# Performance work log

Measured on AMD Instinct MI355X. Metric: run time of the kernel, lower is better.

The kernel has to match this reference:

```python
import jax, jax.numpy as jnp
import numpy as np

B, C, N_IN = 32, 64, 10475
N_OUT = 2619
NNZ = 8 * N_OUT  # ~8 barycentric entries per output vertex


def setup_inputs() -> dict:
    key = jax.random.key(0)
    k1, k2, k3, k4 = jax.random.split(key, 4)
    x = jax.random.normal(k1, (B, C, N_IN), dtype=jnp.float32)
    # Sparse mesh-sampling operator M [N_OUT, N_IN] in COO form,
    # sparsity pattern shared across the whole batch.
    M_rows = jax.random.randint(k2, (NNZ,), 0, N_OUT, dtype=jnp.int32)
    M_cols = jax.random.randint(k3, (NNZ,), 0, N_IN, dtype=jnp.int32)
    M_vals = jax.random.uniform(k4, (NNZ,), dtype=jnp.float32)
    return {"x": x, "M_rows": M_rows, "M_cols": M_cols, "M_vals": M_vals}


def reference(x, M_rows, M_cols, M_vals):
    """Batched spmm: out[b, c, r] = sum_{k: M_rows[k]==r} M_vals[k] * x[b, c, M_cols[k]].

    Equivalent to the torch module: for each batch element, M @ x[b].T, stacked,
    then transposed back to [B, C, N_OUT]. Here the batch loop is fused into a
    single gather + segment_sum that reuses the shared sparsity pattern.
    """
    # Gather source vertex features for every nnz entry: [B, C, NNZ]
    g = x[:, :, M_cols] * M_vals
    # segment_sum reduces over the leading axis -> move nnz to front
    g = jnp.moveaxis(g, 2, 0)                                   # [NNZ, B, C]
    out = jax.ops.segment_sum(g, M_rows, num_segments=N_OUT)    # [N_OUT, B, C]
    return jnp.moveaxis(out, 0, 2)                              # [B, C, N_OUT]
```

## Files before the change

kernel.cpp:

```cpp
#include <hip/hip_runtime.h>
#include <stdint.h>

#define Bdim   32
#define Cdim   64
#define N_IN   10475
#define N_OUT  2619
#define NNZ    (8 * N_OUT)
#define MAIN_BLK 512
#define CHUNK  41
#define SMALL_BLK 256
#define Gpair  2
#define NBLK   (Bdim * Cdim / Gpair)

#define SENT_META 0x03FFC000u

#define OFF_OFFS   10480
#define OFF_ENT    20976
#define OFF_ELAST  (OFF_ENT + 20 * MAIN_BLK * 16)
#define WS_NEEDED  (OFF_ELAST + MAIN_BLK * 8)
#define ENT_U2     ((WS_NEEDED - OFF_ENT) / 8)

__global__ __launch_bounds__(SMALL_BLK) void init_ws(
        int* __restrict__ cursor, uint2* __restrict__ ent2) {
    int i = blockIdx.x * SMALL_BLK + threadIdx.x;
    if (i < N_OUT) cursor[i] = 0;
    if (i < ENT_U2) ent2[i] = make_uint2(SENT_META, 0u);
}

__global__ __launch_bounds__(SMALL_BLK) void hist_rows(
        const int* __restrict__ rows, int* __restrict__ counts) {
    int k = blockIdx.x * SMALL_BLK + threadIdx.x;
    if (k < NNZ) atomicAdd(&counts[rows[k]], 1);
}

__global__ __launch_bounds__(1024) void scan_counts(
        int* __restrict__ counts, int* __restrict__ offsets) {
    __shared__ int wsum[16];
    const int t = threadIdx.x, lane = t & 63, w = t >> 6;
    const int base = t * 3;
    int v0 = (base + 0 < N_OUT) ? counts[base + 0] : 0;
    int v1 = (base + 1 < N_OUT) ? counts[base + 1] : 0;
    int v2 = (base + 2 < N_OUT) ? counts[base + 2] : 0;
    int s = v0 + v1 + v2;
    const int tot = s;
    #pragma unroll
    for (int d = 1; d < 64; d <<= 1) {
        int n = __shfl_up(s, d);
        if (lane >= d) s += n;
    }
    if (lane == 63) wsum[w] = s;
    __syncthreads();
    if (t < 16) {
        int ws_ = wsum[t];
        #pragma unroll
        for (int d = 1; d < 16; d <<= 1) {
            int n = __shfl_up(ws_, d);
            if (t >= d) ws_ += n;
        }
        wsum[t] = ws_;
    }
    __syncthreads();
    int excl = ((w > 0) ? wsum[w - 1] : 0) + (s - tot);
    if (base + 0 <= N_OUT) { offsets[base + 0] = excl; if (base + 0 < N_OUT) counts[base + 0] = excl; }
    excl += v0;
    if (base + 1 <= N_OUT) { offsets[base + 1] = excl; if (base + 1 < N_OUT) counts[base + 1] = excl; }
    excl += v1;
    if (base + 2 <= N_OUT) { offsets[base + 2] = excl; if (base + 2 < N_OUT) counts[base + 2] = excl; }
}

__global__ __launch_bounds__(SMALL_BLK) void scatter_entries(
        const int* __restrict__ rows, const int* __restrict__ cols,
        const float* __restrict__ vals,
        int* __restrict__ cursor, const int* __restrict__ offsets,
        uint2* __restrict__ ent2, uint2* __restrict__ entLast) {
    int k = blockIdx.x * SMALL_BLK + threadIdx.x;
    if (k < NNZ) {
        int r = rows[k];
        int p = atomicAdd(&cursor[r], 1);
        uint32_t flag = (p == offsets[r + 1] - 1) ? 0x80000000u : 0u;
        uint32_t meta = flag | ((uint32_t)r << 14) | (uint32_t)cols[k];
        uint2 e = make_uint2(meta, __float_as_uint(vals[k]));
        int t = p / CHUNK;
        int s = p - t * CHUNK;
        if (s < 40) ent2[(s >> 1) * (MAIN_BLK * 2) + t * 2 + (s & 1)] = e;
        else        entLast[t] = e;
    }
}

__global__ __launch_bounds__(MAIN_BLK) void spmm_g2(
        const float* __restrict__ x,
        const uint4* __restrict__ ent4,
        const uint2* __restrict__ entLast,
        float* __restrict__ out) {
    __shared__ uint32_t xs[N_IN];
    __shared__ float2   out2[N_OUT];
    __shared__ int      wCarryRow[8];
    __shared__ float    wC0[8], wC1[8];

    const int blk  = blockIdx.x;
    const int t    = threadIdx.x, lane = t & 63, w = t >> 6;
    const float* __restrict__ xr0 = x + (size_t)(Gpair * blk) * N_IN;
    const float* __restrict__ xr1 = xr0 + N_IN;

    #pragma unroll 4
    for (int i = t; i < N_IN; i += MAIN_BLK) {
        uint32_t a = __float_as_uint(xr0[i]);
        uint32_t b = __float_as_uint(xr1[i]);
        uint32_t lo = (a + 0x7FFFu + ((a >> 16) & 1u)) >> 16;
        uint32_t hi = (b + 0x7FFFu + ((b >> 16) & 1u)) & 0xFFFF0000u;
        xs[i] = lo | hi;
    }
    #pragma unroll
    for (int i = t; i < N_OUT; i += MAIN_BLK) out2[i] = make_float2(0.f, 0.f);
    __syncthreads();

    float acc0 = 0.f, acc1 = 0.f, f0 = 0.f, f1 = 0.f;
    int firstRow = -1;

#define FEED(meta, vb) do {                                              \
        uint32_t xp = xs[(meta) & 0x3FFFu];                              \
        float v = __uint_as_float(vb);                                   \
        acc0 = fmaf(v, __uint_as_float(xp << 16), acc0);                 \
        acc1 = fmaf(v, __uint_as_float(xp & 0xFFFF0000u), acc1);         \
        if ((int)(meta) < 0) {                                           \
            int row_ = (int)(((meta) >> 14) & 0xFFFu);                   \
            if (firstRow < 0) { firstRow = row_; f0 = acc0; f1 = acc1; } \
            else out2[row_] = make_float2(acc0, acc1);                   \
            acc0 = 0.f; acc1 = 0.f;                                      \
        }                                                                \
    } while (0)

    #pragma unroll
    for (int jb = 0; jb < 5; ++jb) {
        uint4 q0 = ent4[(jb * 4 + 0) * MAIN_BLK + t];
        uint4 q1 = ent4[(jb * 4 + 1) * MAIN_BLK + t];
        uint4 q2 = ent4[(jb * 4 + 2) * MAIN_BLK + t];
        uint4 q3 = ent4[(jb * 4 + 3) * MAIN_BLK + t];
        FEED(q0.x, q0.y); FEED(q0.z, q0.w);
        FEED(q1.x, q1.y); FEED(q1.z, q1.w);
        FEED(q2.x, q2.y); FEED(q2.z, q2.w);
        FEED(q3.x, q3.y); FEED(q3.z, q3.w);
    }
    uint2 el = entLast[t];
    FEED(el.x, el.y);
#undef FEED

    const int   carryRow = (int)((el.x >> 14) & 0xFFFu);
    const float c0 = acc0, c1 = acc1;

    int   pRow = __shfl_up(carryRow, 1);
    float p0   = __shfl_up(c0, 1);
    float p1   = __shfl_up(c1, 1);
    if (lane == 63) { wCarryRow[w] = carryRow; wC0[w] = c0; wC1[w] = c1; }
    __syncthreads();
    if (lane == 0) {
        pRow = (w > 0) ? wCarryRow[w - 1] : -1;
        p0   = (w > 0) ? wC0[w - 1] : 0.f;
        p1   = (w > 0) ? wC1[w - 1] : 0.f;
    }

    if (firstRow >= 0 && firstRow < N_OUT) {
        bool m = (pRow == firstRow);
        out2[firstRow] = make_float2(f0 + (m ? p0 : 0.f),
                                     f1 + (m ? p1 : 0.f));
    }
    __syncthreads();

    float* __restrict__ o0 = out + (size_t)(Gpair * blk) * N_OUT;
    float* __restrict__ o1 = o0 + N_OUT;
    #pragma unroll
    for (int i = t; i < N_OUT; i += MAIN_BLK) {
        float2 vv = out2[i];
        o0[i] = vv.x;
        o1[i] = vv.y;
    }
}

__global__ __launch_bounds__(SMALL_BLK) void spmm_raw(
        const float* __restrict__ x,
        const int* __restrict__ rows,
        const int* __restrict__ cols,
        const float* __restrict__ vals,
        float* __restrict__ out) {
    __shared__ float x_lds[N_IN];
    __shared__ float out_lds[N_OUT];
    const int bc = blockIdx.x;
    const float* __restrict__ xrow = x + (size_t)bc * N_IN;
    for (int i = threadIdx.x; i < N_IN; i += SMALL_BLK) x_lds[i] = xrow[i];
    for (int i = threadIdx.x; i < N_OUT; i += SMALL_BLK) out_lds[i] = 0.0f;
    __syncthreads();
    for (int k = threadIdx.x; k < NNZ; k += SMALL_BLK) {
        atomicAdd(&out_lds[rows[k]], vals[k] * x_lds[cols[k]]);
    }
    __syncthreads();
    float* __restrict__ orow = out + (size_t)bc * N_OUT;
    for (int i = threadIdx.x; i < N_OUT; i += SMALL_BLK) orow[i] = out_lds[i];
}

extern "C" void kernel_launch(void* const* d_in, const int* in_sizes, int n_in,
                              void* d_out, int out_size, void* d_ws, size_t ws_size,
                              hipStream_t stream) {
    const float* x    = (const float*)d_in[0];
    const int*   rows = (const int*)d_in[1];
    const int*   cols = (const int*)d_in[2];
    const float* vals = (const float*)d_in[3];
    float*       out  = (float*)d_out;

    if (ws_size >= (size_t)WS_NEEDED) {
        char*  ws      = (char*)d_ws;
        int*   cursor  = (int*)ws;
        int*   offsets = (int*)(ws + OFF_OFFS);
        uint2* ent2    = (uint2*)(ws + OFF_ENT);
        const uint4* ent4 = (const uint4*)(ws + OFF_ENT);
        uint2* entLast = (uint2*)(ws + OFF_ELAST);

        const int gi = (ENT_U2 + SMALL_BLK - 1) / SMALL_BLK;
        const int gk = (NNZ + SMALL_BLK - 1) / SMALL_BLK;

        init_ws<<<gi, SMALL_BLK, 0, stream>>>(cursor, ent2);
        hist_rows<<<gk, SMALL_BLK, 0, stream>>>(rows, cursor);
        scan_counts<<<1, 1024, 0, stream>>>(cursor, offsets);
        scatter_entries<<<gk, SMALL_BLK, 0, stream>>>(rows, cols, vals, cursor,
                                                      offsets, ent2, entLast);
        spmm_g2<<<NBLK, MAIN_BLK, 0, stream>>>(x, ent4, entLast, out);
    } else {
        spmm_raw<<<Bdim * Cdim, SMALL_BLK, 0, stream>>>(x, rows, cols, vals, out);
    }
}
```

Baseline: 159.3 us.

## Write spmm rows straight to global and fix chunk-boundary carries with atomics

The output staging buffer in shared memory is dropped. Completed rows are stored directly to global memory, and each thread's trailing partial row is merged with a global atomicAdd after a block barrier. This replaces the shuffle and shared-memory carry fix-up. The change cuts LDS use to roughly the x tile, allowing a launch bound of 6 blocks per CU. Entries now encode the column as a byte offset so the LDS address needs no shift, and the next group of entries is prefetched while the current one is consumed. The cost is scattered, uncoalesced global stores and an extra global zeroing pass, in exchange for higher occupancy and less LDS traffic.

```diff
diff --git a/kernel.cpp b/kernel.cpp
--- a/kernel.cpp
+++ b/kernel.cpp
@@ -12,7 +12,7 @@
 #define Gpair  2
 #define NBLK   (Bdim * Cdim / Gpair)
 
-#define SENT_META 0x03FFC000u
+#define SENT_META 0x0FFF0000u
 
 #define OFF_OFFS   10480
 #define OFF_ENT    20976
@@ -78,7 +78,7 @@
         int r = rows[k];
         int p = atomicAdd(&cursor[r], 1);
         uint32_t flag = (p == offsets[r + 1] - 1) ? 0x80000000u : 0u;
-        uint32_t meta = flag | ((uint32_t)r << 14) | (uint32_t)cols[k];
+        uint32_t meta = flag | ((uint32_t)r << 16) | ((uint32_t)cols[k] << 2);
         uint2 e = make_uint2(meta, __float_as_uint(vals[k]));
         int t = p / CHUNK;
         int s = p - t * CHUNK;
@@ -87,20 +87,25 @@
     }
 }
 
-__global__ __launch_bounds__(MAIN_BLK) void spmm_g2(
+__global__ __launch_bounds__(MAIN_BLK, 6) void spmm_g2d(
         const float* __restrict__ x,
         const uint4* __restrict__ ent4,
         const uint2* __restrict__ entLast,
         float* __restrict__ out) {
     __shared__ uint32_t xs[N_IN];
-    __shared__ float2   out2[N_OUT];
-    __shared__ int      wCarryRow[8];
-    __shared__ float    wC0[8], wC1[8];
-
-    const int blk  = blockIdx.x;
-    const int t    = threadIdx.x, lane = t & 63, w = t >> 6;
+
+    const int blk = blockIdx.x;
+    const int t   = threadIdx.x;
     const float* __restrict__ xr0 = x + (size_t)(Gpair * blk) * N_IN;
     const float* __restrict__ xr1 = xr0 + N_IN;
+    float* __restrict__ o0 = out + (size_t)(Gpair * blk) * N_OUT;
+    float* __restrict__ o1 = o0 + N_OUT;
+
+    uint4 c0 = ent4[0 * MAIN_BLK + t];
+    uint4 c1 = ent4[1 * MAIN_BLK + t];
+    uint4 c2 = ent4[2 * MAIN_BLK + t];
+    uint4 c3 = ent4[3 * MAIN_BLK + t];
+    const uint2 el = entLast[t];
 
     #pragma unroll 4
     for (int i = t; i < N_IN; i += MAIN_BLK) {
@@ -111,68 +116,47 @@
         xs[i] = lo | hi;
     }
     #pragma unroll
-    for (int i = t; i < N_OUT; i += MAIN_BLK) out2[i] = make_float2(0.f, 0.f);
-    __syncthreads();
-
-    float acc0 = 0.f, acc1 = 0.f, f0 = 0.f, f1 = 0.f;
-    int firstRow = -1;
+    for (int i = t; i < N_OUT; i += MAIN_BLK) { o0[i] = 0.f; o1[i] = 0.f; }
+    __syncthreads();
+
+    float acc0 = 0.f, acc1 = 0.f;
 
 #define FEED(meta, vb) do {                                              \
-        uint32_t xp = xs[(meta) & 0x3FFFu];                              \
+        uint32_t xp = *(const uint32_t*)((const char*)xs + ((meta) & 0xFFFFu)); \
         float v = __uint_as_float(vb);                                   \
         acc0 = fmaf(v, __uint_as_float(xp << 16), acc0);                 \
         acc1 = fmaf(v, __uint_as_float(xp & 0xFFFF0000u), acc1);         \
         if ((int)(meta) < 0) {                                           \
-            int row_ = (int)(((meta) >> 14) & 0xFFFu);                   \
-            if (firstRow < 0) { firstRow = row_; f0 = acc0; f1 = acc1; } \
-            else out2[row_] = make_float2(acc0, acc1);                   \
+            int row_ = (int)(((meta) >> 16) & 0xFFFu);                   \
+            o0[row_] = acc0;                                             \
+            o1[row_] = acc1;                                             \
             acc0 = 0.f; acc1 = 0.f;                                      \
         }                                                                \
     } while (0)
 
     #pragma unroll
     for (int jb = 0; jb < 5; ++jb) {
-        uint4 q0 = ent4[(jb * 4 + 0) * MAIN_BLK + t];
-        uint4 q1 = ent4[(jb * 4 + 1) * MAIN_BLK + t];
-        uint4 q2 = ent4[(jb * 4 + 2) * MAIN_BLK + t];
-        uint4 q3 = ent4[(jb * 4 + 3) * MAIN_BLK + t];
-        FEED(q0.x, q0.y); FEED(q0.z, q0.w);
-        FEED(q1.x, q1.y); FEED(q1.z, q1.w);
-        FEED(q2.x, q2.y); FEED(q2.z, q2.w);
-        FEED(q3.x, q3.y); FEED(q3.z, q3.w);
-    }
-    uint2 el = entLast[t];
+        uint4 n0, n1, n2, n3;
+        if (jb < 4) {
+            n0 = ent4[((jb + 1) * 4 + 0) * MAIN_BLK + t];
+            n1 = ent4[((jb + 1) * 4 + 1) * MAIN_BLK + t];
+            n2 = ent4[((jb + 1) * 4 + 2) * MAIN_BLK + t];
+            n3 = ent4[((jb + 1) * 4 + 3) * MAIN_BLK + t];
+        }
+        FEED(c0.x, c0.y); FEED(c0.z, c0.w);
+        FEED(c1.x, c1.y); FEED(c1.z, c1.w);
+        FEED(c2.x, c2.y); FEED(c2.z, c2.w);
+        FEED(c3.x, c3.y); FEED(c3.z, c3.w);
+        if (jb < 4) { c0 = n0; c1 = n1; c2 = n2; c3 = n3; }
+    }
     FEED(el.x, el.y);
 #undef FEED
 
-    const int   carryRow = (int)((el.x >> 14) & 0xFFFu);
-    const float c0 = acc0, c1 = acc1;
-
-    int   pRow = __shfl_up(carryRow, 1);
-    float p0   = __shfl_up(c0, 1);
-    float p1   = __shfl_up(c1, 1);
-    if (lane == 63) { wCarryRow[w] = carryRow; wC0[w] = c0; wC1[w] = c1; }
-    __syncthreads();
-    if (lane == 0) {
-        pRow = (w > 0) ? wCarryRow[w - 1] : -1;
-        p0   = (w > 0) ? wC0[w - 1] : 0.f;
-        p1   = (w > 0) ? wC1[w - 1] : 0.f;
-    }
-
-    if (firstRow >= 0 && firstRow < N_OUT) {
-        bool m = (pRow == firstRow);
-        out2[firstRow] = make_float2(f0 + (m ? p0 : 0.f),
-                                     f1 + (m ? p1 : 0.f));
-    }
-    __syncthreads();
-
-    float* __restrict__ o0 = out + (size_t)(Gpair * blk) * N_OUT;
-    float* __restrict__ o1 = o0 + N_OUT;
-    #pragma unroll
-    for (int i = t; i < N_OUT; i += MAIN_BLK) {
-        float2 vv = out2[i];
-        o0[i] = vv.x;
-        o1[i] = vv.y;
+    const int carryRow = (int)((el.x >> 16) & 0xFFFu);
+    __syncthreads();
+    if (carryRow < N_OUT) {
+        atomicAdd(&o0[carryRow], acc0);
+        atomicAdd(&o1[carryRow], acc1);
     }
 }
 
@@ -222,7 +206,7 @@
         scan_counts<<<1, 1024, 0, stream>>>(cursor, offsets);
         scatter_entries<<<gk, SMALL_BLK, 0, stream>>>(rows, cols, vals, cursor,
                                                       offsets, ent2, entLast);
-        spmm_g2<<<NBLK, MAIN_BLK, 0, stream>>>(x, ent4, entLast, out);
+        spmm_g2d<<<NBLK, MAIN_BLK, 0, stream>>>(x, ent4, entLast, out);
     } else {
         spmm_raw<<<Bdim * Cdim, SMALL_BLK, 0, stream>>>(x, rows, cols, vals, out);
     }
```

After: 192.3 us. +20.7%, slower.
